# Kernel optimization log

Hardware: AMD Instinct MI355X
Metric: run time of the kernel (lower is better)

The kernel has to match this reference:

```python
import jax, jax.numpy as jnp
import numpy as np

N, P, VEC, M = 100000, 96, 4, 70000
GROUPS = [27, 8, 8]
K = sum(GROUPS)  # 43
# Replicates the original's use of the LOCAL per-group offset index i_k when
# selecting attention weights in the output accumulation loop.
ATTN_IDX = np.concatenate([np.arange(g) for g in GROUPS]).astype(np.int32)


def setup_inputs() -> dict:
    key = jax.random.key(0)
    ks = jax.random.split(key, 12)
    rng = np.random.default_rng(0)
    # Kernel maps: per offset, M (in_idx, out_idx) pairs; out indices unique per
    # offset (each output point has at most one neighbor at a given offset).
    kmaps = np.stack([
        np.stack([rng.integers(0, N, M), rng.permutation(N)[:M]], axis=1)
        for _ in range(K)
    ]).astype(np.int32)  # [K, M, 2]
    w = lambda k, shape: jax.random.normal(k, shape, jnp.float32) * 0.05
    return dict(
        x=w(ks[0], (N, P)),
        coords=jax.random.uniform(ks[1], (N, 3), jnp.float32, 0.0, 100.0),
        Wq1=w(ks[2], (27, P, P)), gq1=jnp.ones(P), bq1=jnp.zeros(P),
        Wq2=w(ks[3], (27, P, VEC)), gq2=jnp.ones(VEC), bq2=jnp.zeros(VEC),
        Wv=w(ks[4], (27, P, P)), gv=jnp.ones(P), bv=jnp.zeros(P),
        Wp1=w(ks[5], (3, P)), gp1=jnp.ones(P), bp1=jnp.zeros(P),
        Wp2=w(ks[6], (P, VEC)), gp2=jnp.ones(VEC), bp2=jnp.zeros(VEC),
        W1=w(ks[7], (VEC, P)), b1=jnp.zeros(P),
        W2=w(ks[8], (P, VEC)), b2=jnp.zeros(VEC),
        g_out=jnp.ones(P), b_out=jnp.zeros(P),
        kmaps=jnp.asarray(kmaps),
    )


def _bn(x, g, b, eps=1e-5):
    m = x.mean(0)
    v = x.var(0)
    return g * (x - m) * jax.lax.rsqrt(v + eps) + b


def _sparse_conv3(x, W, km27, n):
    # Minkowski kernel-size-3 sparse conv: out[dst] += x[src] @ W[k] per offset.
    def step(acc, kw):
        km, Wk = kw
        return acc.at[km[:, 1]].add(x[km[:, 0]] @ Wk), None
    out, _ = jax.lax.scan(step, jnp.zeros((n, W.shape[-1]), x.dtype), (km27, W))
    return out


def _cbr(x, W, g, b, km27, n):
    return jax.nn.relu(_bn(_sparse_conv3(x, W, km27, n), g, b))


def _forward(x, coords, Wq1, gq1, bq1, Wq2, gq2, bq2, Wv, gv, bv,
             Wp1, gp1, bp1, Wp2, gp2, bp2, W1, b1, W2, b2, g_out, b_out, kmaps):
    n, p = x.shape
    rep = p // VEC  # expand_vec_dim factor
    km27 = kmaps[:27]
    # q branch: two conv3-BN-ReLU stages -> [N, VEC]
    qf = _cbr(_cbr(x, Wq1, gq1, bq1, km27, n), Wq2, gq2, bq2, km27, n)
    # v branch: conv3-BN-ReLU -> [N, P]
    vf = _cbr(x, Wv, gv, bv, km27, n)
    # positional encoding: two 1x1 conv-BN-ReLU on coords -> [N, VEC] -> [N, P]
    pe = jax.nn.relu(_bn(jax.nn.relu(_bn(coords @ Wp1, gp1, bp1)) @ Wp2, gp2, bp2))
    v_f = vf + jnp.repeat(pe, rep, axis=1)

    def attn_step(carry, km):
        src, dst = km[:, 0], km[:, 1]
        # presence mask of offset-k neighbors (scatter of x features, zero elsewhere)
        sm = jnp.zeros((n, p), x.dtype).at[dst].set(x[src])
        mask = jax.lax.stop_gradient((jnp.abs(sm).sum(-1) > 0).astype(x.dtype))  # [N]
        gq = jnp.zeros((n, VEC), x.dtype).at[dst].set(qf[src])
        d = gq - qf * mask[:, None]
        logits = (jax.nn.relu(d @ W1 + b1) @ W2 + b2) * mask[:, None]
        return carry, (logits, mask)

    _, (logits, masks) = jax.lax.scan(attn_step, None, kmaps)  # [K,N,VEC], [K,N]
    attn = jax.nn.softmax(logits, axis=0)  # softmax across the K stacked offsets
    attn_sel = attn[jnp.asarray(ATTN_IDX)]  # replicate local-index selection bug

    def out_step(acc, inp):
        km, mask, a = inp
        nv = jnp.zeros((n, p), x.dtype).at[km[:, 1]].set(v_f[km[:, 0]]) * mask[:, None]
        return acc + nv * jnp.repeat(a, rep, axis=1), None

    out, _ = jax.lax.scan(out_step, jnp.zeros((n, p), x.dtype),
                          (kmaps, masks, attn_sel))
    # out BN + ReLU, residual (inplanes == planes so res = x)
    return jax.nn.relu(_bn(out, g_out, b_out)) + x


def reference(x, coords, Wq1, gq1, bq1, Wq2, gq2, bq2, Wv, gv, bv,
              Wp1, gp1, bp1, Wp2, gp2, bp2, W1, b1, W2, b2, g_out, b_out, kmaps):
    return _forward(x, coords, Wq1, gq1, bq1, Wq2, gq2, bq2, Wv, gv, bv,
                    Wp1, gp1, bp1, Wp2, gp2, bp2, W1, b1, W2, b2,
                    g_out, b_out, kmaps)
```

## Files before the change

kernel.cpp:

```cpp
#include <hip/hip_runtime.h>
#include <math.h>

#define N_  100000
#define P_  96
#define V_  4
#define M_  70000
#define K_  43
#define KC_ 27

typedef unsigned short u16;
typedef __attribute__((ext_vector_type(8))) short bf16x8;
typedef __attribute__((ext_vector_type(4))) float f32x4;

__device__ __forceinline__ u16 f2bf(float f) {
    unsigned int u = __float_as_uint(f);
    u += 0x7fffu + ((u >> 16) & 1u);
    return (u16)(u >> 16);
}
__device__ __forceinline__ float bf2f(u16 h) {
    return __uint_as_float(((unsigned int)h) << 16);
}

__global__ __launch_bounds__(256) void k_build_srcof(const int* __restrict__ km,
                                                     int* __restrict__ srcOf) {
    int idx = blockIdx.x * 256 + threadIdx.x;
    if (idx >= K_ * M_) return;
    int k = idx / M_;
    int e = idx - k * M_;
    const int* p = km + (size_t)(k * M_ + e) * 2;
    srcOf[(size_t)k * N_ + p[1]] = p[0];
}

__global__ __launch_bounds__(256) void k_rowabs_cvt(const float* __restrict__ x,
                                                    float* __restrict__ rowAbs,
                                                    u16* __restrict__ xb) {
    int row = blockIdx.x * 4 + (threadIdx.x >> 6);
    int lane = threadIdx.x & 63;
    if (row >= N_) return;
    const float* xr = x + (size_t)row * 96;
    float s = 0.f;
    for (int j = lane; j < 96; j += 64) {
        float v = xr[j];
        s += fabsf(v);
        xb[(size_t)row * 96 + j] = f2bf(v);
    }
#pragma unroll
    for (int o = 32; o > 0; o >>= 1) s += __shfl_down(s, o, 64);
    if (lane == 0) rowAbs[row] = s;
}

__global__ __launch_bounds__(256) void k_wt96(const float* __restrict__ W,
                                              u16* __restrict__ Wt) {
    int idx = blockIdx.x * 256 + threadIdx.x;
    if (idx >= KC_ * 96 * 96) return;
    int k = idx / 9216, rem = idx - k * 9216, n = rem / 96, j = rem - n * 96;
    Wt[idx] = f2bf(W[(size_t)k * 9216 + j * 96 + n]);
}

__global__ __launch_bounds__(256) void k_wt4(const float* __restrict__ W,
                                             u16* __restrict__ Wt) {
    int idx = blockIdx.x * 256 + threadIdx.x;
    if (idx >= KC_ * 16 * 96) return;
    int k = idx / 1536, rem = idx - k * 1536, n = rem / 96, j = rem - n * 96;
    Wt[idx] = (n < 4) ? f2bf(W[(size_t)k * 384 + j * 4 + n]) : (u16)0;
}

__global__ __launch_bounds__(256) void k_w12b(const float* __restrict__ W1,
                                              const float* __restrict__ W2,
                                              u16* __restrict__ w1b,
                                              u16* __restrict__ w2b) {
    int t = blockIdx.x * 256 + threadIdx.x;
    if (t < 96 * 32) {
        int j = t >> 5, c = t & 31;
        w1b[t] = (c < 4) ? f2bf(W1[c * 96 + j]) : (u16)0;
    }
    if (t < 16 * 96) {
        int n = t / 96, j = t - n * 96;
        w2b[t] = (n < 4) ? f2bf(W2[j * 4 + n]) : (u16)0;
    }
}

__global__ __launch_bounds__(256) void k_conv96_dual(
    const u16* __restrict__ xb, const u16* __restrict__ Wtq,
    const u16* __restrict__ Wtv, const int* __restrict__ srcOf,
    u16* __restrict__ yQ, u16* __restrict__ yV,
    float* __restrict__ statsQ, float* __restrict__ statsV) {
    __shared__ u16 sA[64 * 104];
    __shared__ u16 sBq[96 * 104];
    __shared__ u16 sBv[96 * 104];
    const int r0 = blockIdx.x * 64;
    const int t = threadIdx.x;
    const int wv = t >> 6, lane = t & 63;
    const int m = lane & 15, quad = lane >> 4;
    const int ea = t >> 2, jca = (t & 3) * 3;
    f32x4 accq[6], accv[6];
#pragma unroll
    for (int i = 0; i < 6; i++) {
        accq[i] = (f32x4){0.f, 0.f, 0.f, 0.f};
        accv[i] = (f32x4){0.f, 0.f, 0.f, 0.f};
    }

    for (int k = 0; k < KC_; k++) {
        __syncthreads();
        {
            int r = r0 + ea;
            int src = (r < N_) ? srcOf[(size_t)k * N_ + r] : -1;
            if (src >= 0) {
                const uint4* sp = (const uint4*)(xb + (size_t)src * 96);
#pragma unroll
                for (int i = 0; i < 3; i++)
                    *(uint4*)(sA + ea * 104 + (jca + i) * 8) = sp[jca + i];
            } else {
                uint4 z = make_uint4(0, 0, 0, 0);
#pragma unroll
                for (int i = 0; i < 3; i++)
                    *(uint4*)(sA + ea * 104 + (jca + i) * 8) = z;
            }
        }
        {
            const u16* wkq = Wtq + (size_t)k * 9216;
            const u16* wkv = Wtv + (size_t)k * 9216;
#pragma unroll
            for (int i = 0; i < 5; i++) {
                int c = t + 256 * i;
                if (c < 1152) {
                    int n = c / 12, jc = c - n * 12;
                    *(uint4*)(sBq + n * 104 + jc * 8) = *(const uint4*)(wkq + n * 96 + jc * 8);
                    *(uint4*)(sBv + n * 104 + jc * 8) = *(const uint4*)(wkv + n * 96 + jc * 8);
                }
            }
        }
        __syncthreads();
#pragma unroll
        for (int kk = 0; kk < 3; kk++) {
            bf16x8 af = *(const bf16x8*)(sA + (wv * 16 + m) * 104 + kk * 32 + quad * 8);
#pragma unroll
            for (int nt = 0; nt < 6; nt++) {
                bf16x8 bq = *(const bf16x8*)(sBq + (nt * 16 + m) * 104 + kk * 32 + quad * 8);
                accq[nt] = __builtin_amdgcn_mfma_f32_16x16x32_bf16(af, bq, accq[nt], 0, 0, 0);
                bf16x8 bv = *(const bf16x8*)(sBv + (nt * 16 + m) * 104 + kk * 32 + quad * 8);
                accv[nt] = __builtin_amdgcn_mfma_f32_16x16x32_bf16(af, bv, accv[nt], 0, 0, 0);
            }
        }
    }
#pragma unroll
    for (int nt = 0; nt < 6; nt++) {
#pragma unroll
        for (int rg = 0; rg < 4; rg++) {
            int r = r0 + wv * 16 + quad * 4 + rg;
            if (r < N_) {
                yQ[(size_t)r * 96 + nt * 16 + m] = f2bf(accq[nt][rg]);
                yV[(size_t)r * 96 + nt * 16 + m] = f2bf(accv[nt][rg]);
            }
        }
    }
    __syncthreads();
    float* sred = (float*)sA;
#pragma unroll
    for (int pass = 0; pass < 2; pass++) {
        f32x4* acc = pass ? accv : accq;
        float* st = pass ? statsV : statsQ;
        float sv[6], qv[6];
#pragma unroll
        for (int nt = 0; nt < 6; nt++) {
            f32x4 a = acc[nt];
            sv[nt] = a[0] + a[1] + a[2] + a[3];
            qv[nt] = a[0] * a[0] + a[1] * a[1] + a[2] * a[2] + a[3] * a[3];
            sv[nt] += __shfl_xor(sv[nt], 16, 64);
            sv[nt] += __shfl_xor(sv[nt], 32, 64);
            qv[nt] += __shfl_xor(qv[nt], 16, 64);
            qv[nt] += __shfl_xor(qv[nt], 32, 64);
        }
        if (quad == 0) {
#pragma unroll
            for (int nt = 0; nt < 6; nt++) {
                int ch = nt * 16 + m;
                sred[wv * 192 + ch] = sv[nt];
                sred[wv * 192 + 96 + ch] = qv[nt];
            }
        }
        __syncthreads();
        if (t < 192) {
            float tot = sred[t] + sred[192 + t] + sred[384 + t] + sred[576 + t];
            atomicAdd(&st[t], tot);
        }
        __syncthreads();
    }
}

__global__ __launch_bounds__(256) void k_conv4_mfma(
    const u16* __restrict__ xbA, const u16* __restrict__ Wt4,
    const int* __restrict__ srcOf, float* __restrict__ qf) {
    __shared__ u16 sA[128 * 104];
    __shared__ u16 sB[16 * 104];
    const int r0 = blockIdx.x * 128;
    const int t = threadIdx.x;
    const int wv = t >> 6, lane = t & 63;
    const int m = lane & 15, quad = lane >> 4;
    const int ea = t >> 1, jca = (t & 1) * 6;
    f32x4 acc[2];
    acc[0] = (f32x4){0.f, 0.f, 0.f, 0.f};
    acc[1] = (f32x4){0.f, 0.f, 0.f, 0.f};
    for (int k = 0; k < KC_; k++) {
        __syncthreads();
        {
            int r = r0 + ea;
            int src = (r < N_) ? srcOf[(size_t)k * N_ + r] : -1;
            if (src >= 0) {
                const uint4* sp = (const uint4*)(xbA + (size_t)src * 96);
#pragma unroll
                for (int i = 0; i < 6; i++)
                    *(uint4*)(sA + ea * 104 + (jca + i) * 8) = sp[jca + i];
            } else {
                uint4 z = make_uint4(0, 0, 0, 0);
#pragma unroll
                for (int i = 0; i < 6; i++)
                    *(uint4*)(sA + ea * 104 + (jca + i) * 8) = z;
            }
        }
        if (t < 192) {
            int n = t / 12, jc = t - (t / 12) * 12;
            *(uint4*)(sB + n * 104 + jc * 8) =
                *(const uint4*)(Wt4 + (size_t)k * 1536 + n * 96 + jc * 8);
        }
        __syncthreads();
#pragma unroll
        for (int kk = 0; kk < 3; kk++) {
            bf16x8 bfr = *(const bf16x8*)(sB + m * 104 + kk * 32 + quad * 8);
#pragma unroll
            for (int rt = 0; rt < 2; rt++) {
                bf16x8 af = *(const bf16x8*)(sA + ((wv * 2 + rt) * 16 + m) * 104 + kk * 32 + quad * 8);
                acc[rt] = __builtin_amdgcn_mfma_f32_16x16x32_bf16(af, bfr, acc[rt], 0, 0, 0);
            }
        }
    }
    if (m < 4) {
#pragma unroll
        for (int rt = 0; rt < 2; rt++)
#pragma unroll
            for (int rg = 0; rg < 4; rg++) {
                int r = r0 + (wv * 2 + rt) * 16 + quad * 4 + rg;
                if (r < N_) qf[(size_t)r * 4 + m] = acc[rt][rg];
            }
    }
}

__global__ __launch_bounds__(192) void k_bnstats96(const float* __restrict__ xin,
                                                   float* __restrict__ stats) {
    __shared__ float sS[192], sQ[192];
    int t = threadIdx.x;
    int ch = t % 96, half = t / 96;
    float s = 0.f, q = 0.f;
    for (int r = blockIdx.x * 2 + half; r < N_; r += gridDim.x * 2) {
        float v = xin[(size_t)r * 96 + ch];
        s += v; q += v * v;
    }
    sS[t] = s; sQ[t] = q;
    __syncthreads();
    if (t < 96) {
        atomicAdd(&stats[ch], sS[t] + sS[t + 96]);
        atomicAdd(&stats[96 + ch], sQ[t] + sQ[t + 96]);
    }
}

__global__ __launch_bounds__(256) void k_bnstats4(const float* __restrict__ xin,
                                                  float* __restrict__ stats) {
    __shared__ float sS[256], sQ[256];
    int t = threadIdx.x;
    int c = t & 3, sub = t >> 2;
    float s = 0.f, q = 0.f;
    for (int r = blockIdx.x * 64 + sub; r < N_; r += gridDim.x * 64) {
        float v = xin[(size_t)r * 4 + c];
        s += v; q += v * v;
    }
    sS[t] = s; sQ[t] = q;
    __syncthreads();
    for (int off = 128; off >= 4; off >>= 1) {
        if (t < off) { sS[t] += sS[t + off]; sQ[t] += sQ[t + off]; }
        __syncthreads();
    }
    if (t < 4) {
        atomicAdd(&stats[t], sS[t]);
        atomicAdd(&stats[96 + t], sQ[t]);
    }
}

template <int C, int MODE>
__global__ __launch_bounds__(256) void k_bnapply(float* __restrict__ y,
                                                 const float* __restrict__ stats,
                                                 const float* __restrict__ g,
                                                 const float* __restrict__ b,
                                                 const float* __restrict__ aux) {
    int idx = blockIdx.x * 256 + threadIdx.x;
    if (idx >= N_ * C) return;
    int ch = idx % C;
    float mean = stats[ch] * (1.f / N_);
    float var = stats[96 + ch] * (1.f / N_) - mean * mean;
    float scale = g[ch] * rsqrtf(fmaxf(var, 0.f) + 1e-5f);
    float v = (y[idx] - mean) * scale + b[ch];
    v = fmaxf(v, 0.f);
    if (MODE == 2) v += aux[idx];
    y[idx] = v;
}

template <int MODE>
__global__ __launch_bounds__(256) void k_bnapply96_b2b(
    const u16* __restrict__ yin, const float* __restrict__ stats,
    const float* __restrict__ g, const float* __restrict__ b,
    const float* __restrict__ aux, u16* __restrict__ yout) {
    int idx = blockIdx.x * 256 + threadIdx.x;
    if (idx >= N_ * 96) return;
    int ch = idx % 96;
    float mean = stats[ch] * (1.f / N_);
    float var = stats[96 + ch] * (1.f / N_) - mean * mean;
    float scale = g[ch] * rsqrtf(fmaxf(var, 0.f) + 1e-5f);
    float v = (bf2f(yin[idx]) - mean) * scale + b[ch];
    v = fmaxf(v, 0.f);
    if (MODE == 1) { int r = idx / 96; v += aux[(size_t)r * 4 + (ch / 24)]; }
    yout[idx] = f2bf(v);
}

__global__ __launch_bounds__(256) void k_pe1(const float* __restrict__ coords,
                                             const float* __restrict__ Wp1,
                                             float* __restrict__ out) {
    int idx = blockIdx.x * 256 + threadIdx.x;
    if (idx >= N_ * 96) return;
    int r = idx / 96, ch = idx - r * 96;
    float c0 = coords[r * 3], c1 = coords[r * 3 + 1], c2 = coords[r * 3 + 2];
    out[idx] = c0 * Wp1[ch] + c1 * Wp1[96 + ch] + c2 * Wp1[192 + ch];
}

__global__ __launch_bounds__(256) void k_pe2(const float* __restrict__ hin,
                                             const float* __restrict__ Wp2,
                                             float* __restrict__ out) {
    int idx = blockIdx.x * 256 + threadIdx.x;
    if (idx >= N_ * 4) return;
    int r = idx / 4, c = idx & 3;
    const float* hr = hin + (size_t)r * 96;
    float acc = 0.f;
#pragma unroll 4
    for (int j = 0; j < 96; j++) acc += hr[j] * Wp2[j * 4 + c];
    out[idx] = acc;
}

__global__ __launch_bounds__(256) void k_attn_logits_mfma(
    const float* __restrict__ qf, const int* __restrict__ srcOf,
    const float* __restrict__ rowAbs,
    const u16* __restrict__ w1b, const float* __restrict__ b1,
    const u16* __restrict__ w2b, const float* __restrict__ b2,
    u16* __restrict__ wb) {
    __shared__ u16 hbuf[4][16 * 104];
    __shared__ u16 slogb[32][176];
    __shared__ u16 smk16[32][44];
    const int t = threadIdx.x;
    const int wv = t >> 6, lane = t & 63;
    const int col = lane & 15, quad = lane >> 4;
    const int r0 = blockIdx.x * 32;

    bf16x8 w1f[6];
    float b1v[6];
#pragma unroll
    for (int nt = 0; nt < 6; nt++) {
        w1f[nt] = *(const bf16x8*)(w1b + (nt * 16 + col) * 32 + quad * 8);
        b1v[nt] = b1[nt * 16 + col];
    }
    bf16x8 w2f[3];
#pragma unroll
    for (int kk = 0; kk < 3; kk++)
        w2f[kk] = *(const bf16x8*)(w2b + col * 96 + kk * 32 + quad * 8);
    float b2v = b2[col & 3];

    u16* hb = hbuf[wv];
    for (int tt = 0; tt < 22; tt++) {
        int tileBase = (wv * 22 + tt) * 16;
        bf16x8 af = (bf16x8){0, 0, 0, 0, 0, 0, 0, 0};
        if (quad == 0) {
            int P = tileBase + col;
            int rL = P / 44, k = P - rL * 44;
            int kc = (k < 43) ? k : 42;
            int r = r0 + rL;
            int s = srcOf[(size_t)kc * N_ + r];
            if (k == 43) s = -1;
            int sc = (s >= 0) ? s : 0;
            float mk = (s >= 0 && rowAbs[sc] > 0.f) ? 1.f : 0.f;
            float4 qs = *(const float4*)(qf + (size_t)sc * 4);
            float4 qr = *(const float4*)(qf + (size_t)r * 4);
            af[0] = (short)f2bf((qs.x - qr.x) * mk);
            af[1] = (short)f2bf((qs.y - qr.y) * mk);
            af[2] = (short)f2bf((qs.z - qr.z) * mk);
            af[3] = (short)f2bf((qs.w - qr.w) * mk);
            if (k < 43) smk16[rL][k] = (u16)(mk > 0.f ? 1 : 0);
        }
        f32x4 c1[6];
#pragma unroll
        for (int nt = 0; nt < 6; nt++) {
            c1[nt] = (f32x4){0.f, 0.f, 0.f, 0.f};
            c1[nt] = __builtin_amdgcn_mfma_f32_16x16x32_bf16(af, w1f[nt], c1[nt], 0, 0, 0);
        }
#pragma unroll
        for (int nt = 0; nt < 6; nt++) {
#pragma unroll
            for (int rg = 0; rg < 4; rg++) {
                float h = fmaxf(c1[nt][rg] + b1v[nt], 0.f);
                hb[(quad * 4 + rg) * 104 + nt * 16 + col] = f2bf(h);
            }
        }
        f32x4 acc2 = (f32x4){0.f, 0.f, 0.f, 0.f};
#pragma unroll
        for (int kk = 0; kk < 3; kk++) {
            bf16x8 a2 = *(const bf16x8*)(hb + col * 104 + kk * 32 + quad * 8);
            acc2 = __builtin_amdgcn_mfma_f32_16x16x32_bf16(a2, w2f[kk], acc2, 0, 0, 0);
        }
        if (col < 4) {
#pragma unroll
            for (int rg = 0; rg < 4; rg++) {
                int P = tileBase + quad * 4 + rg;
                int rL = P / 44, k = P - rL * 44;
                if (k < 43) {
                    float mval = (float)smk16[rL][k];
                    slogb[rL][k * 4 + col] = f2bf((acc2[rg] + b2v) * mval);
                }
            }
        }
    }
    __syncthreads();

    if (t < 128) {
        int rL = t >> 2, c = t & 3;
        float mx = 0.f;
        for (int k = 0; k < K_; k++) mx = fmaxf(mx, bf2f(slogb[rL][k * 4 + c]));
        float den = 0.f;
        for (int k = 0; k < K_; k++) den += __expf(bf2f(slogb[rL][k * 4 + c]) - mx);
        float inv = 1.f / den;
        for (int k = 0; k < K_; k++)
            slogb[rL][k * 4 + c] = f2bf(__expf(bf2f(slogb[rL][k * 4 + c]) - mx) * inv);
    }
    __syncthreads();

    for (int p = t; p < 32 * 43; p += 256) {
        int rL = p / 43, k = p - rL * 43;
        int idxk = (k < 27) ? k : ((k < 35) ? (k - 27) : (k - 35));
        u16 mk = smk16[rL][k];
        ushort4 wout = make_ushort4(0, 0, 0, 0);
        if (mk) {
            wout.x = slogb[rL][idxk * 4 + 0];
            wout.y = slogb[rL][idxk * 4 + 1];
            wout.z = slogb[rL][idxk * 4 + 2];
            wout.w = slogb[rL][idxk * 4 + 3];
        }
        *(ushort4*)(wb + ((size_t)(r0 + rL) * 44 + k) * 4) = wout;
    }
}

__global__ __launch_bounds__(256) void k_attn_gather(
    const u16* __restrict__ vfb, const u16* __restrict__ wb,
    const int* __restrict__ srcOf, float* __restrict__ out) {
    int idx = blockIdx.x * 256 + threadIdx.x;
    int r = idx / 24, c4 = idx - r * 24;
    if (r >= N_) return;
    int cg = c4 / 6;
    const u16* wrow = wb + (size_t)r * 176 + cg;
    float a0 = 0.f, a1 = 0.f, a2 = 0.f, a3 = 0.f;
    for (int k = 0; k < K_; k++) {
        int s = srcOf[(size_t)k * N_ + r];
        float w = bf2f(wrow[(size_t)k * 4]);
        w = (s >= 0) ? w : 0.f;
        int sc = (s >= 0) ? s : 0;
        ushort4 v = *(const ushort4*)(vfb + (size_t)sc * 96 + c4 * 4);
        a0 += w * bf2f(v.x);
        a1 += w * bf2f(v.y);
        a2 += w * bf2f(v.z);
        a3 += w * bf2f(v.w);
    }
    *(float4*)(out + (size_t)r * 96 + c4 * 4) = make_float4(a0, a1, a2, a3);
}

extern "C" void kernel_launch(void* const* d_in, const int* in_sizes, int n_in,
                              void* d_out, int out_size, void* d_ws, size_t ws_size,
                              hipStream_t stream) {
    const float* x      = (const float*)d_in[0];
    const float* coords = (const float*)d_in[1];
    const float* Wq1 = (const float*)d_in[2];
    const float* gq1 = (const float*)d_in[3];
    const float* bq1 = (const float*)d_in[4];
    const float* Wq2 = (const float*)d_in[5];
    const float* gq2 = (const float*)d_in[6];
    const float* bq2 = (const float*)d_in[7];
    const float* Wv  = (const float*)d_in[8];
    const float* gv  = (const float*)d_in[9];
    const float* bv  = (const float*)d_in[10];
    const float* Wp1 = (const float*)d_in[11];
    const float* gp1 = (const float*)d_in[12];
    const float* bp1 = (const float*)d_in[13];
    const float* Wp2 = (const float*)d_in[14];
    const float* gp2 = (const float*)d_in[15];
    const float* bp2 = (const float*)d_in[16];
    const float* W1  = (const float*)d_in[17];
    const float* b1  = (const float*)d_in[18];
    const float* W2  = (const float*)d_in[19];
    const float* b2  = (const float*)d_in[20];
    const float* g_out = (const float*)d_in[21];
    const float* b_out = (const float*)d_in[22];
    const int* kmaps = (const int*)d_in[23];
    float* out = (float*)d_out;

    char* ws = (char*)d_ws;
    int*   srcOf  = (int*)ws;
    float* rowAbs = (float*)(ws + 17200000);
    u16*   xb     = (u16*)(ws + 17600000);
    u16*   bufQb  = (u16*)(ws + 36800000);
    u16*   bufVb  = (u16*)(ws + 56000000);
    u16*   bufAb  = (u16*)(ws + 75200000);
    u16*   vfb    = (u16*)(ws + 75200000);
    float* pescr  = (float*)(ws + 17600000);
    u16*   wbuf   = (u16*)(ws + 17600000);
    float* qf     = (float*)(ws + 94400000);
    float* peb    = (float*)(ws + 96000000);
    u16*   Wq1t   = (u16*)(ws + 97600000);
    u16*   Wvt    = (u16*)(ws + 98097664);
    u16*   Wq2t   = (u16*)(ws + 98595328);
    u16*   w1b    = (u16*)(ws + 98678272);
    u16*   w2b    = (u16*)(ws + 98684416);
    float* stats  = (float*)(ws + 98687488);

    hipMemsetAsync(srcOf, 0xFF, (size_t)K_ * N_ * 4, stream);
    hipMemsetAsync(stats, 0, 6 * 192 * 4, stream);

    k_build_srcof<<<(K_ * M_ + 255) / 256, 256, 0, stream>>>(kmaps, srcOf);
    k_rowabs_cvt<<<N_ / 4, 256, 0, stream>>>(x, rowAbs, xb);
    k_wt96<<<(KC_ * 9216 + 255) / 256, 256, 0, stream>>>(Wq1, Wq1t);
    k_wt96<<<(KC_ * 9216 + 255) / 256, 256, 0, stream>>>(Wv, Wvt);
    k_wt4<<<(KC_ * 1536 + 255) / 256, 256, 0, stream>>>(Wq2, Wq2t);
    k_w12b<<<12, 256, 0, stream>>>(W1, W2, w1b, w2b);

    const int cb96 = (N_ + 63) / 64;
    const int cb4  = (N_ + 127) / 128;
    const int eb96 = N_ * 96 / 256;
    const int eb4  = (N_ * 4 + 255) / 256;

    k_conv96_dual<<<cb96, 256, 0, stream>>>(xb, Wq1t, Wvt, srcOf, bufQb, bufVb,
                                            stats + 0 * 192, stats + 4 * 192);

    k_bnapply96_b2b<0><<<eb96, 256, 0, stream>>>(bufQb, stats + 0 * 192, gq1, bq1, nullptr, bufAb);
    k_conv4_mfma<<<cb4, 256, 0, stream>>>(bufAb, Wq2t, srcOf, qf);
    k_bnstats4<<<512, 256, 0, stream>>>(qf, stats + 1 * 192);
    k_bnapply<4, 0><<<eb4, 256, 0, stream>>>(qf, stats + 1 * 192, gq2, bq2, nullptr);

    k_pe1<<<eb96, 256, 0, stream>>>(coords, Wp1, pescr);
    k_bnstats96<<<512, 192, 0, stream>>>(pescr, stats + 2 * 192);
    k_bnapply<96, 0><<<eb96, 256, 0, stream>>>(pescr, stats + 2 * 192, gp1, bp1, nullptr);
    k_pe2<<<eb4, 256, 0, stream>>>(pescr, Wp2, peb);
    k_bnstats4<<<512, 256, 0, stream>>>(peb, stats + 3 * 192);
    k_bnapply<4, 0><<<eb4, 256, 0, stream>>>(peb, stats + 3 * 192, gp2, bp2, nullptr);

    k_bnapply96_b2b<1><<<eb96, 256, 0, stream>>>(bufVb, stats + 4 * 192, gv, bv, peb, vfb);

    k_attn_logits_mfma<<<N_ / 32, 256, 0, stream>>>(qf, srcOf, rowAbs, w1b, b1, w2b, b2, wbuf);
    k_attn_gather<<<(N_ * 24) / 256, 256, 0, stream>>>(vfb, wbuf, srcOf, out);

    k_bnstats96<<<512, 192, 0, stream>>>(out, stats + 5 * 192);
    k_bnapply<96, 2><<<eb96, 256, 0, stream>>>(out, stats + 5 * 192, g_out, b_out, x);
}
```

Before: 1.068 ms.

## Enlarge dual conv tile to 192 rows with 32x32 MFMA and direct LDS weight loads

```diff
diff --git a/kernel.cpp b/kernel.cpp
--- a/kernel.cpp
+++ b/kernel.cpp
@@ -11,6 +11,7 @@
 typedef unsigned short u16;
 typedef __attribute__((ext_vector_type(8))) short bf16x8;
 typedef __attribute__((ext_vector_type(4))) float f32x4;
+typedef __attribute__((ext_vector_type(16))) float f32x16;
 
 __device__ __forceinline__ u16 f2bf(float f) {
     unsigned int u = __float_as_uint(f);
@@ -19,6 +20,12 @@
 }
 __device__ __forceinline__ float bf2f(u16 h) {
     return __uint_as_float(((unsigned int)h) << 16);
+}
+
+__device__ __forceinline__ void gl_lds16(const u16* g, u16* l) {
+    __builtin_amdgcn_global_load_lds(
+        (const __attribute__((address_space(1))) void*)g,
+        (__attribute__((address_space(3))) void*)l, 16, 0, 0);
 }
 
 __global__ __launch_bounds__(256) void k_build_srcof(const int* __restrict__ km,
@@ -49,12 +56,12 @@
     if (lane == 0) rowAbs[row] = s;
 }
 
-__global__ __launch_bounds__(256) void k_wt96(const float* __restrict__ W,
-                                              u16* __restrict__ Wt) {
+__global__ __launch_bounds__(256) void k_wt96p(const float* __restrict__ W,
+                                               u16* __restrict__ Wp) {
     int idx = blockIdx.x * 256 + threadIdx.x;
     if (idx >= KC_ * 96 * 96) return;
     int k = idx / 9216, rem = idx - k * 9216, n = rem / 96, j = rem - n * 96;
-    Wt[idx] = f2bf(W[(size_t)k * 9216 + j * 96 + n]);
+    Wp[(size_t)k * 10240 + n * 104 + j] = f2bf(W[(size_t)k * 9216 + j * 96 + n]);
 }
 
 __global__ __launch_bounds__(256) void k_wt4(const float* __restrict__ W,
@@ -80,108 +87,102 @@
     }
 }
 
-__global__ __launch_bounds__(256) void k_conv96_dual(
-    const u16* __restrict__ xb, const u16* __restrict__ Wtq,
-    const u16* __restrict__ Wtv, const int* __restrict__ srcOf,
+__global__ __launch_bounds__(384, 3) void k_conv96_dual(
+    const u16* __restrict__ xb, const u16* __restrict__ Wqp,
+    const u16* __restrict__ Wvp, const int* __restrict__ srcOf,
     u16* __restrict__ yQ, u16* __restrict__ yV,
     float* __restrict__ statsQ, float* __restrict__ statsV) {
-    __shared__ u16 sA[64 * 104];
-    __shared__ u16 sBq[96 * 104];
-    __shared__ u16 sBv[96 * 104];
-    const int r0 = blockIdx.x * 64;
+    __shared__ u16 sA[192 * 104];
+    __shared__ u16 sBq[10240];
+    __shared__ u16 sBv[10240];
+    const int r0 = blockIdx.x * 192;
     const int t = threadIdx.x;
-    const int wv = t >> 6, lane = t & 63;
-    const int m = lane & 15, quad = lane >> 4;
-    const int ea = t >> 2, jca = (t & 3) * 3;
-    f32x4 accq[6], accv[6];
-#pragma unroll
-    for (int i = 0; i < 6; i++) {
-        accq[i] = (f32x4){0.f, 0.f, 0.f, 0.f};
-        accv[i] = (f32x4){0.f, 0.f, 0.f, 0.f};
+    const int wv = t / 64, lane = t & 63;
+    const int n32 = lane & 31, half = lane >> 5;
+    const int ea = t >> 1, jca = (t & 1) * 6;
+    f32x16 accq[3], accv[3];
+#pragma unroll
+    for (int i = 0; i < 3; i++) {
+#pragma unroll
+        for (int j = 0; j < 16; j++) { accq[i][j] = 0.f; accv[i][j] = 0.f; }
     }
 
     for (int k = 0; k < KC_; k++) {
         __syncthreads();
+        {
+            const u16* gq = Wqp + (size_t)k * 10240;
+            const u16* gv = Wvp + (size_t)k * 10240;
+            for (int i = wv; i < 40; i += 6) {
+                int mv = (i >= 20);
+                int off = (mv ? i - 20 : i) * 512 + lane * 8;
+                gl_lds16((mv ? gv : gq) + off, (mv ? (u16*)sBv : (u16*)sBq) + off);
+            }
+        }
         {
             int r = r0 + ea;
             int src = (r < N_) ? srcOf[(size_t)k * N_ + r] : -1;
             if (src >= 0) {
                 const uint4* sp = (const uint4*)(xb + (size_t)src * 96);
 #pragma unroll
-                for (int i = 0; i < 3; i++)
+                for (int i = 0; i < 6; i++)
                     *(uint4*)(sA + ea * 104 + (jca + i) * 8) = sp[jca + i];
             } else {
                 uint4 z = make_uint4(0, 0, 0, 0);
 #pragma unroll
-                for (int i = 0; i < 3; i++)
+                for (int i = 0; i < 6; i++)
                     *(uint4*)(sA + ea * 104 + (jca + i) * 8) = z;
             }
         }
-        {
-            const u16* wkq = Wtq + (size_t)k * 9216;
-            const u16* wkv = Wtv + (size_t)k * 9216;
-#pragma unroll
-            for (int i = 0; i < 5; i++) {
-                int c = t + 256 * i;
-                if (c < 1152) {
-                    int n = c / 12, jc = c - n * 12;
-                    *(uint4*)(sBq + n * 104 + jc * 8) = *(const uint4*)(wkq + n * 96 + jc * 8);
-                    *(uint4*)(sBv + n * 104 + jc * 8) = *(const uint4*)(wkv + n * 96 + jc * 8);
-                }
-            }
-        }
-        __syncthreads();
-#pragma unroll
-        for (int kk = 0; kk < 3; kk++) {
-            bf16x8 af = *(const bf16x8*)(sA + (wv * 16 + m) * 104 + kk * 32 + quad * 8);
-#pragma unroll
-            for (int nt = 0; nt < 6; nt++) {
-                bf16x8 bq = *(const bf16x8*)(sBq + (nt * 16 + m) * 104 + kk * 32 + quad * 8);
-                accq[nt] = __builtin_amdgcn_mfma_f32_16x16x32_bf16(af, bq, accq[nt], 0, 0, 0);
-                bf16x8 bv = *(const bf16x8*)(sBv + (nt * 16 + m) * 104 + kk * 32 + quad * 8);
-                accv[nt] = __builtin_amdgcn_mfma_f32_16x16x32_bf16(af, bv, accv[nt], 0, 0, 0);
-            }
-        }
-    }
-#pragma unroll
-    for (int nt = 0; nt < 6; nt++) {
-#pragma unroll
-        for (int rg = 0; rg < 4; rg++) {
-            int r = r0 + wv * 16 + quad * 4 + rg;
+        __syncthreads();
+#pragma unroll
+        for (int ks = 0; ks < 6; ks++) {
+            bf16x8 af = *(const bf16x8*)(sA + (wv * 32 + n32) * 104 + ks * 16 + half * 8);
+#pragma unroll
+            for (int nt = 0; nt < 3; nt++) {
+                bf16x8 bq = *(const bf16x8*)(sBq + (nt * 32 + n32) * 104 + ks * 16 + half * 8);
+                accq[nt] = __builtin_amdgcn_mfma_f32_32x32x16_bf16(af, bq, accq[nt], 0, 0, 0);
+                bf16x8 bv = *(const bf16x8*)(sBv + (nt * 32 + n32) * 104 + ks * 16 + half * 8);
+                accv[nt] = __builtin_amdgcn_mfma_f32_32x32x16_bf16(af, bv, accv[nt], 0, 0, 0);
+            }
+        }
+    }
+#pragma unroll
+    for (int nt = 0; nt < 3; nt++) {
+#pragma unroll
+        for (int reg = 0; reg < 16; reg++) {
+            int row = (reg & 3) + 8 * (reg >> 2) + 4 * half;
+            int r = r0 + wv * 32 + row;
             if (r < N_) {
-                yQ[(size_t)r * 96 + nt * 16 + m] = f2bf(accq[nt][rg]);
-                yV[(size_t)r * 96 + nt * 16 + m] = f2bf(accv[nt][rg]);
+                yQ[(size_t)r * 96 + nt * 32 + n32] = f2bf(accq[nt][reg]);
+                yV[(size_t)r * 96 + nt * 32 + n32] = f2bf(accv[nt][reg]);
             }
         }
     }
     __syncthreads();
     float* sred = (float*)sA;
-#pragma unroll
     for (int pass = 0; pass < 2; pass++) {
-        f32x4* acc = pass ? accv : accq;
+        f32x16* acc = pass ? accv : accq;
         float* st = pass ? statsV : statsQ;
-        float sv[6], qv[6];
-#pragma unroll
-        for (int nt = 0; nt < 6; nt++) {
-            f32x4 a = acc[nt];
-            sv[nt] = a[0] + a[1] + a[2] + a[3];
-            qv[nt] = a[0] * a[0] + a[1] * a[1] + a[2] * a[2] + a[3] * a[3];
-            sv[nt] += __shfl_xor(sv[nt], 16, 64);
-            sv[nt] += __shfl_xor(sv[nt], 32, 64);
-            qv[nt] += __shfl_xor(qv[nt], 16, 64);
-            qv[nt] += __shfl_xor(qv[nt], 32, 64);
-        }
-        if (quad == 0) {
-#pragma unroll
-            for (int nt = 0; nt < 6; nt++) {
-                int ch = nt * 16 + m;
-                sred[wv * 192 + ch] = sv[nt];
-                sred[wv * 192 + 96 + ch] = qv[nt];
+#pragma unroll
+        for (int nt = 0; nt < 3; nt++) {
+            float sv = 0.f, qv = 0.f;
+#pragma unroll
+            for (int reg = 0; reg < 16; reg++) {
+                float a = acc[nt][reg];
+                sv += a; qv += a * a;
+            }
+            sv += __shfl_xor(sv, 32, 64);
+            qv += __shfl_xor(qv, 32, 64);
+            if (half == 0) {
+                sred[wv * 192 + nt * 32 + n32] = sv;
+                sred[wv * 192 + 96 + nt * 32 + n32] = qv;
             }
         }
         __syncthreads();
         if (t < 192) {
-            float tot = sred[t] + sred[192 + t] + sred[384 + t] + sred[576 + t];
+            float tot = 0.f;
+#pragma unroll
+            for (int w = 0; w < 6; w++) tot += sred[w * 192 + t];
             atomicAdd(&st[t], tot);
         }
         __syncthreads();
@@ -516,30 +517,30 @@
     u16*   wbuf   = (u16*)(ws + 17600000);
     float* qf     = (float*)(ws + 94400000);
     float* peb    = (float*)(ws + 96000000);
-    u16*   Wq1t   = (u16*)(ws + 97600000);
-    u16*   Wvt    = (u16*)(ws + 98097664);
-    u16*   Wq2t   = (u16*)(ws + 98595328);
-    u16*   w1b    = (u16*)(ws + 98678272);
-    u16*   w2b    = (u16*)(ws + 98684416);
-    float* stats  = (float*)(ws + 98687488);
+    u16*   Wq1p   = (u16*)(ws + 97600000);
+    u16*   Wvp    = (u16*)(ws + 98152960);
+    u16*   Wq2t   = (u16*)(ws + 98705920);
+    u16*   w1b    = (u16*)(ws + 98788864);
+    u16*   w2b    = (u16*)(ws + 98795008);
+    float* stats  = (float*)(ws + 98798080);
 
     hipMemsetAsync(srcOf, 0xFF, (size_t)K_ * N_ * 4, stream);
     hipMemsetAsync(stats, 0, 6 * 192 * 4, stream);
 
     k_build_srcof<<<(K_ * M_ + 255) / 256, 256, 0, stream>>>(kmaps, srcOf);
     k_rowabs_cvt<<<N_ / 4, 256, 0, stream>>>(x, rowAbs, xb);
-    k_wt96<<<(KC_ * 9216 + 255) / 256, 256, 0, stream>>>(Wq1, Wq1t);
-    k_wt96<<<(KC_ * 9216 + 255) / 256, 256, 0, stream>>>(Wv, Wvt);
+    k_wt96p<<<(KC_ * 9216 + 255) / 256, 256, 0, stream>>>(Wq1, Wq1p);
+    k_wt96p<<<(KC_ * 9216 + 255) / 256, 256, 0, stream>>>(Wv, Wvp);
     k_wt4<<<(KC_ * 1536 + 255) / 256, 256, 0, stream>>>(Wq2, Wq2t);
     k_w12b<<<12, 256, 0, stream>>>(W1, W2, w1b, w2b);
 
-    const int cb96 = (N_ + 63) / 64;
+    const int cbD  = (N_ + 191) / 192;
     const int cb4  = (N_ + 127) / 128;
     const int eb96 = N_ * 96 / 256;
     const int eb4  = (N_ * 4 + 255) / 256;
 
-    k_conv96_dual<<<cb96, 256, 0, stream>>>(xb, Wq1t, Wvt, srcOf, bufQb, bufVb,
-                                            stats + 0 * 192, stats + 4 * 192);
+    k_conv96_dual<<<cbD, 384, 0, stream>>>(xb, Wq1p, Wvp, srcOf, bufQb, bufVb,
+                                           stats + 0 * 192, stats + 4 * 192);
 
     k_bnapply96_b2b<0><<<eb96, 256, 0, stream>>>(bufQb, stats + 0 * 192, gq1, bq1, nullptr, bufAb);
     k_conv4_mfma<<<cb4, 256, 0, stream>>>(bufAb, Wq2t, srcOf, qf);
```

Result: faster. 996.0 us (-6.7%).
